# Optimization experiments

Hardware: AMD Instinct MI355X
Metric: run time of the kernel (lower is better)

The kernel has to match this reference:

```python
import jax, jax.numpy as jnp
import numpy as np

B, S, H, D = 2, 4096, 32, 128  # batch, seq_len, num_heads, key_size
BLOCK = 128                     # block_size (S must be divisible)


def setup_inputs() -> dict:
    key = jax.random.key(0)
    kq, kk, kv = jax.random.split(key, 3)
    q = jax.random.normal(kq, (B, S, H * D), dtype=jnp.float32)
    k = jax.random.normal(kk, (B, S, H * D), dtype=jnp.float32)
    v = jax.random.normal(kv, (B, S, H * D), dtype=jnp.float32)
    return {"q": q, "k": k, "v": v}


def reference(q, k, v):
    batch, seq_len, _ = q.shape
    nb = seq_len // BLOCK  # num_blocks
    # reshape to [B, nb, block, H, D]
    qb = q.reshape(batch, nb, BLOCK, H, D)
    kb = k.reshape(batch, nb, BLOCK, H, D)
    vb = v.reshape(batch, nb, BLOCK, H, D)
    scale = np.float32(1.0 / np.sqrt(D))
    # Faithful to original einsum '...hd,...kd->...hk': contraction is over d
    # with (nb, block) as batch dims, so attention runs over the HEAD axis (g).
    logits = jnp.einsum("bnshd,bnsgd->bnshg", qb, kb) * scale  # [B,nb,block,H,H]
    w = jax.nn.softmax(logits, axis=-1)
    out = jnp.einsum("bnshg,bnsgd->bnshd", w, vb)  # [B,nb,block,H,D]
    return out.reshape(batch, seq_len, H * D)
```

## Files before the change

kernel.cpp:

```cpp
#include <hip/hip_runtime.h>


typedef __bf16 bf16x8 __attribute__((ext_vector_type(8)));
typedef __bf16 bf16x2 __attribute__((ext_vector_type(2)));
typedef float  f32x4  __attribute__((ext_vector_type(4)));

static constexpr float kScale = 0.08838834764831845f;

typedef const __attribute__((address_space(1))) unsigned int* gas_ptr;
typedef __attribute__((address_space(3))) unsigned int* las_ptr;

__device__ inline bf16x8 to_bf16x8(f32x4 a, f32x4 b) {
  bf16x8 f;
  f[0] = (__bf16)a[0]; f[1] = (__bf16)a[1];
  f[2] = (__bf16)a[2]; f[3] = (__bf16)a[3];
  f[4] = (__bf16)b[0]; f[5] = (__bf16)b[1];
  f[6] = (__bf16)b[2]; f[7] = (__bf16)b[3];
  return f;
}

__global__ __launch_bounds__(256, 2) void attn_headwise(
    const float* __restrict__ q, const float* __restrict__ k,
    const float* __restrict__ v, float* __restrict__ out, int ntok) {
  const int wave = threadIdx.x >> 6;
  const int lane = threadIdx.x & 63;
  const int lr   = lane & 15;
  const int G    = lane >> 4;

  const long token = (long)blockIdx.x * 4 + wave;
  if (token >= ntok) return;
  const float* qt = q + token * 4096;
  const float* kt = k + token * 4096;
  const float* vt = v + token * 4096;
  float*       ot = out + token * 4096;

  __shared__ __align__(16) float        vbuf[4][32 * 128];
  __shared__ __align__(16) unsigned int pbuf[4][32 * 16];
  float*        vl = vbuf[wave];
  unsigned int* pl = pbuf[wave];

  f32x4 kraw[4][2][2], qraw[4][2][2];
  #pragma unroll
  for (int kk = 0; kk < 4; ++kk)
    #pragma unroll
    for (int t = 0; t < 2; ++t) {
      const float* pk = kt + (16 * t + lr) * 128 + 32 * kk + 8 * G;
      kraw[kk][t][0] = *(const f32x4*)pk;
      kraw[kk][t][1] = *(const f32x4*)(pk + 4);
      const float* pq = qt + (16 * t + lr) * 128 + 32 * kk + 8 * G;
      qraw[kk][t][0] = *(const f32x4*)pq;
      qraw[kk][t][1] = *(const f32x4*)(pq + 4);
    }

  {
    const float* vsrc = vt + lane * 4;
    #pragma unroll
    for (int i = 0; i < 16; ++i)
      __builtin_amdgcn_global_load_lds((gas_ptr)(vsrc + i * 256),
                                       (las_ptr)(vl + i * 256), 16, 0, 0);
  }

  f32x4 acc[2][2];
  acc[0][0] = 0.f; acc[0][1] = 0.f; acc[1][0] = 0.f; acc[1][1] = 0.f;
  #pragma unroll
  for (int kk = 0; kk < 4; ++kk) {
    bf16x8 af[2], bq[2];
    #pragma unroll
    for (int t = 0; t < 2; ++t) {
      af[t] = to_bf16x8(kraw[kk][t][0], kraw[kk][t][1]);
      bq[t] = to_bf16x8(qraw[kk][t][0], qraw[kk][t][1]);
    }
    #pragma unroll
    for (int gi = 0; gi < 2; ++gi)
      #pragma unroll
      for (int hj = 0; hj < 2; ++hj)
        acc[gi][hj] = __builtin_amdgcn_mfma_f32_16x16x32_bf16(
            af[gi], bq[hj], acc[gi][hj], 0, 0, 0);
  }

  #pragma unroll
  for (int hj = 0; hj < 2; ++hj) {
    float m = acc[0][hj][0];
    #pragma unroll
    for (int gi = 0; gi < 2; ++gi)
      #pragma unroll
      for (int r = 0; r < 4; ++r) m = fmaxf(m, acc[gi][hj][r]);
    m = fmaxf(m, __shfl_xor(m, 16, 64));
    m = fmaxf(m, __shfl_xor(m, 32, 64));

    float pv[2][4];
    float s = 0.f;
    #pragma unroll
    for (int gi = 0; gi < 2; ++gi)
      #pragma unroll
      for (int r = 0; r < 4; ++r) {
        float e = __expf((acc[gi][hj][r] - m) * kScale);
        pv[gi][r] = e;
        s += e;
      }
    s += __shfl_xor(s, 16, 64);
    s += __shfl_xor(s, 32, 64);
    float inv = 1.0f / s;

    #pragma unroll
    for (int gi = 0; gi < 2; ++gi)
      #pragma unroll
      for (int mp = 0; mp < 2; ++mp) {
        bf16x2 t;
        t[0] = (__bf16)(pv[gi][2 * mp]     * inv);
        t[1] = (__bf16)(pv[gi][2 * mp + 1] * inv);
        pl[(16 * hj + lr) * 16 + 8 * gi + 2 * G + mp] =
            __builtin_bit_cast(unsigned int, t);
      }
  }

  bf16x8 pf[2];
  #pragma unroll
  for (int ht = 0; ht < 2; ++ht)
    pf[ht] = *(const bf16x8*)&pl[(16 * ht + lr) * 16 + 4 * G];

  asm volatile("s_waitcnt vmcnt(0)" ::: "memory");
  f32x4 zero = 0.f;
  #pragma unroll
  for (int dt = 0; dt < 8; ++dt) {
    bf16x8 vf;
    #pragma unroll
    for (int e = 0; e < 8; ++e)
      vf[e] = (__bf16)vl[(8 * G + e) * 128 + 16 * dt + lr];
    f32x4 o0 = __builtin_amdgcn_mfma_f32_16x16x32_bf16(vf, pf[0], zero, 0, 0, 0);
    f32x4 o1 = __builtin_amdgcn_mfma_f32_16x16x32_bf16(vf, pf[1], zero, 0, 0, 0);
    *(f32x4*)&ot[lr * 128 + 16 * dt + 4 * G]        = o0;
    *(f32x4*)&ot[(16 + lr) * 128 + 16 * dt + 4 * G] = o1;
  }
}

extern "C" void kernel_launch(void* const* d_in, const int* in_sizes, int n_in,
                              void* d_out, int out_size, void* d_ws, size_t ws_size,
                              hipStream_t stream) {
  const float* q = (const float*)d_in[0];
  const float* k = (const float*)d_in[1];
  const float* v = (const float*)d_in[2];
  float* out = (float*)d_out;
  int ntok = in_sizes[0] / 4096;
  int grid = (ntok + 3) / 4;
  hipLaunchKernelGGL(attn_headwise, dim3(grid), dim3(256), 0, stream,
                     q, k, v, out, ntok);
}
```

Before: 113.3 us.

## Process multiple tokens per wave with register double-buffered prefetch

Each wave now handles several tokens in a grid-strided loop. While the current token is computed, it prefetches the next token's Q/K and V into registers, with sched_barriers placed so the loads overlap the MFMA and softmax work. V no longer goes through LDS via global_load_lds. Instead it is read straight into registers with scalar-per-element loads, and the P buffer row stride is padded to 20 to cut bank conflicts. The register footprint grows a lot (double-buffered raw fp32 Q/K/V), which risks spilling or lower occupancy, and the V loads become strided 4-byte accesses that coalesce less well.

```diff
diff --git a/kernel.cpp b/kernel.cpp
--- a/kernel.cpp
+++ b/kernel.cpp
@@ -6,9 +6,7 @@
 typedef float  f32x4  __attribute__((ext_vector_type(4)));
 
 static constexpr float kScale = 0.08838834764831845f;
-
-typedef const __attribute__((address_space(1))) unsigned int* gas_ptr;
-typedef __attribute__((address_space(3))) unsigned int* las_ptr;
+static constexpr int kTPW = 4;
 
 __device__ inline bf16x8 to_bf16x8(f32x4 a, f32x4 b) {
   bf16x8 f;
@@ -26,111 +24,133 @@
   const int lane = threadIdx.x & 63;
   const int lr   = lane & 15;
   const int G    = lane >> 4;
+  const int NW   = gridDim.x * 4;
+  const long wid = (long)blockIdx.x * 4 + wave;
 
-  const long token = (long)blockIdx.x * 4 + wave;
-  if (token >= ntok) return;
-  const float* qt = q + token * 4096;
-  const float* kt = k + token * 4096;
-  const float* vt = v + token * 4096;
-  float*       ot = out + token * 4096;
-
-  __shared__ __align__(16) float        vbuf[4][32 * 128];
-  __shared__ __align__(16) unsigned int pbuf[4][32 * 16];
-  float*        vl = vbuf[wave];
+  __shared__ __align__(16) unsigned int pbuf[4][32 * 20];
   unsigned int* pl = pbuf[wave];
 
-  f32x4 kraw[4][2][2], qraw[4][2][2];
-  #pragma unroll
-  for (int kk = 0; kk < 4; ++kk)
+  f32x4 kraw[2][4][2][2], qraw[2][4][2][2];
+  float vraw[2][8][8];
+
+  auto loadQK = [&](int buf, long t) {
+    const float* kt = k + t * 4096;
+    const float* qt = q + t * 4096;
     #pragma unroll
-    for (int t = 0; t < 2; ++t) {
-      const float* pk = kt + (16 * t + lr) * 128 + 32 * kk + 8 * G;
-      kraw[kk][t][0] = *(const f32x4*)pk;
-      kraw[kk][t][1] = *(const f32x4*)(pk + 4);
-      const float* pq = qt + (16 * t + lr) * 128 + 32 * kk + 8 * G;
-      qraw[kk][t][0] = *(const f32x4*)pq;
-      qraw[kk][t][1] = *(const f32x4*)(pq + 4);
-    }
+    for (int kk = 0; kk < 4; ++kk)
+      #pragma unroll
+      for (int tt = 0; tt < 2; ++tt) {
+        const float* pk = kt + (16 * tt + lr) * 128 + 32 * kk + 8 * G;
+        kraw[buf][kk][tt][0] = *(const f32x4*)pk;
+        kraw[buf][kk][tt][1] = *(const f32x4*)(pk + 4);
+        const float* pq = qt + (16 * tt + lr) * 128 + 32 * kk + 8 * G;
+        qraw[buf][kk][tt][0] = *(const f32x4*)pq;
+        qraw[buf][kk][tt][1] = *(const f32x4*)(pq + 4);
+      }
+  };
+  auto loadV = [&](int buf, long t) {
+    const float* vt = v + t * 4096;
+    #pragma unroll
+    for (int dt = 0; dt < 8; ++dt)
+      #pragma unroll
+      for (int e = 0; e < 8; ++e)
+        vraw[buf][dt][e] = vt[(8 * G + e) * 128 + 16 * dt + lr];
+  };
 
-  {
-    const float* vsrc = vt + lane * 4;
-    #pragma unroll
-    for (int i = 0; i < 16; ++i)
-      __builtin_amdgcn_global_load_lds((gas_ptr)(vsrc + i * 256),
-                                       (las_ptr)(vl + i * 256), 16, 0, 0);
-  }
-
-  f32x4 acc[2][2];
-  acc[0][0] = 0.f; acc[0][1] = 0.f; acc[1][0] = 0.f; acc[1][1] = 0.f;
-  #pragma unroll
-  for (int kk = 0; kk < 4; ++kk) {
-    bf16x8 af[2], bq[2];
-    #pragma unroll
-    for (int t = 0; t < 2; ++t) {
-      af[t] = to_bf16x8(kraw[kk][t][0], kraw[kk][t][1]);
-      bq[t] = to_bf16x8(qraw[kk][t][0], qraw[kk][t][1]);
-    }
-    #pragma unroll
-    for (int gi = 0; gi < 2; ++gi)
-      #pragma unroll
-      for (int hj = 0; hj < 2; ++hj)
-        acc[gi][hj] = __builtin_amdgcn_mfma_f32_16x16x32_bf16(
-            af[gi], bq[hj], acc[gi][hj], 0, 0, 0);
-  }
+  long tok = wid;
+  if (tok < ntok) { loadQK(0, tok); loadV(0, tok); }
 
   #pragma unroll
-  for (int hj = 0; hj < 2; ++hj) {
-    float m = acc[0][hj][0];
-    #pragma unroll
-    for (int gi = 0; gi < 2; ++gi)
+  for (int it = 0; it < kTPW; ++it) {
+    const int cur = it & 1, nxt = cur ^ 1;
+    const long tn = tok + NW;
+    if (tok < ntok) {
+      float* ot = out + tok * 4096;
+
+      bf16x8 kf[4][2], qf[4][2];
       #pragma unroll
-      for (int r = 0; r < 4; ++r) m = fmaxf(m, acc[gi][hj][r]);
-    m = fmaxf(m, __shfl_xor(m, 16, 64));
-    m = fmaxf(m, __shfl_xor(m, 32, 64));
+      for (int kk = 0; kk < 4; ++kk)
+        #pragma unroll
+        for (int tt = 0; tt < 2; ++tt) {
+          kf[kk][tt] = to_bf16x8(kraw[cur][kk][tt][0], kraw[cur][kk][tt][1]);
+          qf[kk][tt] = to_bf16x8(qraw[cur][kk][tt][0], qraw[cur][kk][tt][1]);
+        }
 
-    float pv[2][4];
-    float s = 0.f;
-    #pragma unroll
-    for (int gi = 0; gi < 2; ++gi)
+      bf16x8 vf[8];
       #pragma unroll
-      for (int r = 0; r < 4; ++r) {
-        float e = __expf((acc[gi][hj][r] - m) * kScale);
-        pv[gi][r] = e;
-        s += e;
+      for (int dt = 0; dt < 8; ++dt)
+        #pragma unroll
+        for (int e = 0; e < 8; ++e)
+          vf[dt][e] = (__bf16)vraw[cur][dt][e];
+
+      if (it + 1 < kTPW && tn < ntok) loadQK(nxt, tn);
+      __builtin_amdgcn_sched_barrier(0);
+
+      f32x4 acc[2][2];
+      acc[0][0] = 0.f; acc[0][1] = 0.f; acc[1][0] = 0.f; acc[1][1] = 0.f;
+      #pragma unroll
+      for (int kk = 0; kk < 4; ++kk)
+        #pragma unroll
+        for (int gi = 0; gi < 2; ++gi)
+          #pragma unroll
+          for (int hj = 0; hj < 2; ++hj)
+            acc[gi][hj] = __builtin_amdgcn_mfma_f32_16x16x32_bf16(
+                kf[kk][gi], qf[kk][hj], acc[gi][hj], 0, 0, 0);
+
+      #pragma unroll
+      for (int hj = 0; hj < 2; ++hj) {
+        float m = acc[0][hj][0];
+        #pragma unroll
+        for (int gi = 0; gi < 2; ++gi)
+          #pragma unroll
+          for (int r = 0; r < 4; ++r) m = fmaxf(m, acc[gi][hj][r]);
+        m = fmaxf(m, __shfl_xor(m, 16, 64));
+        m = fmaxf(m, __shfl_xor(m, 32, 64));
+
+        float pv[2][4];
+        float s = 0.f;
+        #pragma unroll
+        for (int gi = 0; gi < 2; ++gi)
+          #pragma unroll
+          for (int r = 0; r < 4; ++r) {
+            float e = __expf((acc[gi][hj][r] - m) * kScale);
+            pv[gi][r] = e;
+            s += e;
+          }
+        s += __shfl_xor(s, 16, 64);
+        s += __shfl_xor(s, 32, 64);
+        float inv = 1.0f / s;
+
+        #pragma unroll
+        for (int gi = 0; gi < 2; ++gi)
+          #pragma unroll
+          for (int mp = 0; mp < 2; ++mp) {
+            bf16x2 t2;
+            t2[0] = (__bf16)(pv[gi][2 * mp]     * inv);
+            t2[1] = (__bf16)(pv[gi][2 * mp + 1] * inv);
+            pl[(16 * hj + lr) * 20 + 8 * gi + 2 * G + mp] =
+                __builtin_bit_cast(unsigned int, t2);
+          }
       }
-    s += __shfl_xor(s, 16, 64);
-    s += __shfl_xor(s, 32, 64);
-    float inv = 1.0f / s;
 
-    #pragma unroll
-    for (int gi = 0; gi < 2; ++gi)
+      bf16x8 pf[2];
       #pragma unroll
-      for (int mp = 0; mp < 2; ++mp) {
-        bf16x2 t;
-        t[0] = (__bf16)(pv[gi][2 * mp]     * inv);
-        t[1] = (__bf16)(pv[gi][2 * mp + 1] * inv);
-        pl[(16 * hj + lr) * 16 + 8 * gi + 2 * G + mp] =
-            __builtin_bit_cast(unsigned int, t);
+      for (int ht = 0; ht < 2; ++ht)
+        pf[ht] = *(const bf16x8*)&pl[(16 * ht + lr) * 20 + 4 * G];
+
+      if (it + 1 < kTPW && tn < ntok) loadV(nxt, tn);
+      __builtin_amdgcn_sched_barrier(0);
+
+      f32x4 zero = 0.f;
+      #pragma unroll
+      for (int dt = 0; dt < 8; ++dt) {
+        f32x4 o0 = __builtin_amdgcn_mfma_f32_16x16x32_bf16(vf[dt], pf[0], zero, 0, 0, 0);
+        f32x4 o1 = __builtin_amdgcn_mfma_f32_16x16x32_bf16(vf[dt], pf[1], zero, 0, 0, 0);
+        *(f32x4*)&ot[lr * 128 + 16 * dt + 4 * G]        = o0;
+        *(f32x4*)&ot[(16 + lr) * 128 + 16 * dt + 4 * G] = o1;
       }
-  }
-
-  bf16x8 pf[2];
-  #pragma unroll
-  for (int ht = 0; ht < 2; ++ht)
-    pf[ht] = *(const bf16x8*)&pl[(16 * ht + lr) * 16 + 4 * G];
-
-  asm volatile("s_waitcnt vmcnt(0)" ::: "memory");
-  f32x4 zero = 0.f;
-  #pragma unroll
-  for (int dt = 0; dt < 8; ++dt) {
-    bf16x8 vf;
-    #pragma unroll
-    for (int e = 0; e < 8; ++e)
-      vf[e] = (__bf16)vl[(8 * G + e) * 128 + 16 * dt + lr];
-    f32x4 o0 = __builtin_amdgcn_mfma_f32_16x16x32_bf16(vf, pf[0], zero, 0, 0, 0);
-    f32x4 o1 = __builtin_amdgcn_mfma_f32_16x16x32_bf16(vf, pf[1], zero, 0, 0, 0);
-    *(f32x4*)&ot[lr * 128 + 16 * dt + 4 * G]        = o0;
-    *(f32x4*)&ot[(16 + lr) * 128 + 16 * dt + 4 * G] = o1;
+    }
+    tok = tn;
   }
 }
 
@@ -142,7 +162,7 @@
   const float* v = (const float*)d_in[2];
   float* out = (float*)d_out;
   int ntok = in_sizes[0] / 4096;
-  int grid = (ntok + 3) / 4;
+  int grid = (ntok + 4 * kTPW - 1) / (4 * kTPW);
   hipLaunchKernelGGL(attn_headwise, dim3(grid), dim3(256), 0, stream,
                      q, k, v, out, ntok);
 }
```

Result: slower. 289.8 us (+155.7%).

## Pipeline four tokens per single-wave block with double-buffered V prefetch

Applied to the files above, without the earlier changes.

Each block becomes a single wave that handles four consecutive tokens in sequence. While the current token's softmax and PV product run, the next token's Q and K are prefetched into registers and its V into a second LDS buffer, with a partial vmcnt wait so those loads overlap compute. The aim is to hide global-load latency in what is essentially a bandwidth-bound kernel. The P scratch row stride is padded to 20 words to reduce LDS bank conflicts. The cost is fewer resident waves per CU, because of the larger per-wave LDS footprint and 64-thread blocks, which may reduce latency hiding from occupancy.

```diff
diff --git a/kernel.cpp b/kernel.cpp
--- a/kernel.cpp
+++ b/kernel.cpp
@@ -6,6 +6,7 @@
 typedef float  f32x4  __attribute__((ext_vector_type(4)));
 
 static constexpr float kScale = 0.08838834764831845f;
+static constexpr int kTPW = 4;
 
 typedef const __attribute__((address_space(1))) unsigned int* gas_ptr;
 typedef __attribute__((address_space(3))) unsigned int* las_ptr;
@@ -19,118 +20,137 @@
   return f;
 }
 
-__global__ __launch_bounds__(256, 2) void attn_headwise(
+__global__ __launch_bounds__(64) void attn_headwise(
     const float* __restrict__ q, const float* __restrict__ k,
     const float* __restrict__ v, float* __restrict__ out, int ntok) {
-  const int wave = threadIdx.x >> 6;
-  const int lane = threadIdx.x & 63;
+  const int lane = threadIdx.x;
   const int lr   = lane & 15;
   const int G    = lane >> 4;
+  const long base = (long)blockIdx.x * kTPW;
 
-  const long token = (long)blockIdx.x * 4 + wave;
-  if (token >= ntok) return;
-  const float* qt = q + token * 4096;
-  const float* kt = k + token * 4096;
-  const float* vt = v + token * 4096;
-  float*       ot = out + token * 4096;
-
-  __shared__ __align__(16) float        vbuf[4][32 * 128];
-  __shared__ __align__(16) unsigned int pbuf[4][32 * 16];
-  float*        vl = vbuf[wave];
-  unsigned int* pl = pbuf[wave];
+  __shared__ __align__(16) float        vbuf[2][32 * 128];
+  __shared__ __align__(16) unsigned int pbuf[32 * 20];
 
   f32x4 kraw[4][2][2], qraw[4][2][2];
-  #pragma unroll
-  for (int kk = 0; kk < 4; ++kk)
+
+  auto clampTok = [&](long t) { return t < (long)ntok ? t : (long)ntok - 1; };
+
+  auto issueQK = [&](long t) {
+    const float* kt = k + t * 4096;
+    const float* qt = q + t * 4096;
     #pragma unroll
-    for (int t = 0; t < 2; ++t) {
-      const float* pk = kt + (16 * t + lr) * 128 + 32 * kk + 8 * G;
-      kraw[kk][t][0] = *(const f32x4*)pk;
-      kraw[kk][t][1] = *(const f32x4*)(pk + 4);
-      const float* pq = qt + (16 * t + lr) * 128 + 32 * kk + 8 * G;
-      qraw[kk][t][0] = *(const f32x4*)pq;
-      qraw[kk][t][1] = *(const f32x4*)(pq + 4);
-    }
-
-  {
-    const float* vsrc = vt + lane * 4;
+    for (int kk = 0; kk < 4; ++kk)
+      #pragma unroll
+      for (int tt = 0; tt < 2; ++tt) {
+        const float* pk = kt + (16 * tt + lr) * 128 + 32 * kk + 8 * G;
+        kraw[kk][tt][0] = *(const f32x4*)pk;
+        kraw[kk][tt][1] = *(const f32x4*)(pk + 4);
+        const float* pq = qt + (16 * tt + lr) * 128 + 32 * kk + 8 * G;
+        qraw[kk][tt][0] = *(const f32x4*)pq;
+        qraw[kk][tt][1] = *(const f32x4*)(pq + 4);
+      }
+  };
+  auto issueV = [&](long t, int buf) {
+    const float* vsrc = v + t * 4096 + lane * 4;
+    float*       vdst = vbuf[buf];
     #pragma unroll
     for (int i = 0; i < 16; ++i)
       __builtin_amdgcn_global_load_lds((gas_ptr)(vsrc + i * 256),
-                                       (las_ptr)(vl + i * 256), 16, 0, 0);
-  }
+                                       (las_ptr)(vdst + i * 256), 16, 0, 0);
+  };
 
-  f32x4 acc[2][2];
-  acc[0][0] = 0.f; acc[0][1] = 0.f; acc[1][0] = 0.f; acc[1][1] = 0.f;
-  #pragma unroll
-  for (int kk = 0; kk < 4; ++kk) {
-    bf16x8 af[2], bq[2];
-    #pragma unroll
-    for (int t = 0; t < 2; ++t) {
-      af[t] = to_bf16x8(kraw[kk][t][0], kraw[kk][t][1]);
-      bq[t] = to_bf16x8(qraw[kk][t][0], qraw[kk][t][1]);
-    }
-    #pragma unroll
-    for (int gi = 0; gi < 2; ++gi)
-      #pragma unroll
-      for (int hj = 0; hj < 2; ++hj)
-        acc[gi][hj] = __builtin_amdgcn_mfma_f32_16x16x32_bf16(
-            af[gi], bq[hj], acc[gi][hj], 0, 0, 0);
-  }
+  issueQK(clampTok(base));
+  issueV(clampTok(base), 0);
 
   #pragma unroll
-  for (int hj = 0; hj < 2; ++hj) {
-    float m = acc[0][hj][0];
+  for (int it = 0; it < kTPW; ++it) {
+    const long tok = clampTok(base + it);
+    float* ot = out + tok * 4096;
+
+    f32x4 acc[2][2];
+    acc[0][0] = 0.f; acc[0][1] = 0.f; acc[1][0] = 0.f; acc[1][1] = 0.f;
     #pragma unroll
-    for (int gi = 0; gi < 2; ++gi)
+    for (int kk = 0; kk < 4; ++kk) {
+      bf16x8 kf[2], qf[2];
       #pragma unroll
-      for (int r = 0; r < 4; ++r) m = fmaxf(m, acc[gi][hj][r]);
-    m = fmaxf(m, __shfl_xor(m, 16, 64));
-    m = fmaxf(m, __shfl_xor(m, 32, 64));
+      for (int tt = 0; tt < 2; ++tt) {
+        kf[tt] = to_bf16x8(kraw[kk][tt][0], kraw[kk][tt][1]);
+        qf[tt] = to_bf16x8(qraw[kk][tt][0], qraw[kk][tt][1]);
+      }
+      #pragma unroll
+      for (int gi = 0; gi < 2; ++gi)
+        #pragma unroll
+        for (int hj = 0; hj < 2; ++hj)
+          acc[gi][hj] = __builtin_amdgcn_mfma_f32_16x16x32_bf16(
+              kf[gi], qf[hj], acc[gi][hj], 0, 0, 0);
+    }
 
-    float pv[2][4];
-    float s = 0.f;
-    #pragma unroll
-    for (int gi = 0; gi < 2; ++gi)
-      #pragma unroll
-      for (int r = 0; r < 4; ++r) {
-        float e = __expf((acc[gi][hj][r] - m) * kScale);
-        pv[gi][r] = e;
-        s += e;
-      }
-    s += __shfl_xor(s, 16, 64);
-    s += __shfl_xor(s, 32, 64);
-    float inv = 1.0f / s;
+    if (it + 1 < kTPW) {
+      issueQK(clampTok(base + it + 1));
+      issueV(clampTok(base + it + 1), (it + 1) & 1);
+    }
+    __builtin_amdgcn_sched_barrier(0);
 
     #pragma unroll
-    for (int gi = 0; gi < 2; ++gi)
+    for (int hj = 0; hj < 2; ++hj) {
+      float m = acc[0][hj][0];
       #pragma unroll
-      for (int mp = 0; mp < 2; ++mp) {
-        bf16x2 t;
-        t[0] = (__bf16)(pv[gi][2 * mp]     * inv);
-        t[1] = (__bf16)(pv[gi][2 * mp + 1] * inv);
-        pl[(16 * hj + lr) * 16 + 8 * gi + 2 * G + mp] =
-            __builtin_bit_cast(unsigned int, t);
-      }
-  }
+      for (int gi = 0; gi < 2; ++gi)
+        #pragma unroll
+        for (int r = 0; r < 4; ++r) m = fmaxf(m, acc[gi][hj][r]);
+      m = fmaxf(m, __shfl_xor(m, 16, 64));
+      m = fmaxf(m, __shfl_xor(m, 32, 64));
 
-  bf16x8 pf[2];
-  #pragma unroll
-  for (int ht = 0; ht < 2; ++ht)
-    pf[ht] = *(const bf16x8*)&pl[(16 * ht + lr) * 16 + 4 * G];
+      float pv[2][4];
+      float s = 0.f;
+      #pragma unroll
+      for (int gi = 0; gi < 2; ++gi)
+        #pragma unroll
+        for (int r = 0; r < 4; ++r) {
+          float e = __expf((acc[gi][hj][r] - m) * kScale);
+          pv[gi][r] = e;
+          s += e;
+        }
+      s += __shfl_xor(s, 16, 64);
+      s += __shfl_xor(s, 32, 64);
+      float inv = 1.0f / s;
 
-  asm volatile("s_waitcnt vmcnt(0)" ::: "memory");
-  f32x4 zero = 0.f;
-  #pragma unroll
-  for (int dt = 0; dt < 8; ++dt) {
-    bf16x8 vf;
+      #pragma unroll
+      for (int gi = 0; gi < 2; ++gi)
+        #pragma unroll
+        for (int mp = 0; mp < 2; ++mp) {
+          bf16x2 t2;
+          t2[0] = (__bf16)(pv[gi][2 * mp]     * inv);
+          t2[1] = (__bf16)(pv[gi][2 * mp + 1] * inv);
+          pbuf[(16 * hj + lr) * 20 + 8 * gi + 2 * G + mp] =
+              __builtin_bit_cast(unsigned int, t2);
+        }
+    }
+    bf16x8 pf[2];
     #pragma unroll
-    for (int e = 0; e < 8; ++e)
-      vf[e] = (__bf16)vl[(8 * G + e) * 128 + 16 * dt + lr];
-    f32x4 o0 = __builtin_amdgcn_mfma_f32_16x16x32_bf16(vf, pf[0], zero, 0, 0, 0);
-    f32x4 o1 = __builtin_amdgcn_mfma_f32_16x16x32_bf16(vf, pf[1], zero, 0, 0, 0);
-    *(f32x4*)&ot[lr * 128 + 16 * dt + 4 * G]        = o0;
-    *(f32x4*)&ot[(16 + lr) * 128 + 16 * dt + 4 * G] = o1;
+    for (int ht = 0; ht < 2; ++ht)
+      pf[ht] = *(const bf16x8*)&pbuf[(16 * ht + lr) * 20 + 4 * G];
+
+    if (it + 1 < kTPW) {
+      asm volatile("s_waitcnt vmcnt(48)" ::: "memory");
+    } else {
+      asm volatile("s_waitcnt vmcnt(0)" ::: "memory");
+    }
+    __builtin_amdgcn_sched_barrier(0);
+
+    const float* vl = vbuf[it & 1];
+    f32x4 zero = 0.f;
+    #pragma unroll
+    for (int dt = 0; dt < 8; ++dt) {
+      bf16x8 vf;
+      #pragma unroll
+      for (int e = 0; e < 8; ++e)
+        vf[e] = (__bf16)vl[(8 * G + e) * 128 + 16 * dt + lr];
+      f32x4 o0 = __builtin_amdgcn_mfma_f32_16x16x32_bf16(vf, pf[0], zero, 0, 0, 0);
+      f32x4 o1 = __builtin_amdgcn_mfma_f32_16x16x32_bf16(vf, pf[1], zero, 0, 0, 0);
+      *(f32x4*)&ot[lr * 128 + 16 * dt + 4 * G]        = o0;
+      *(f32x4*)&ot[(16 + lr) * 128 + 16 * dt + 4 * G] = o1;
+    }
   }
 }
 
@@ -142,7 +162,7 @@
   const float* v = (const float*)d_in[2];
   float* out = (float*)d_out;
   int ntok = in_sizes[0] / 4096;
-  int grid = (ntok + 3) / 4;
-  hipLaunchKernelGGL(attn_headwise, dim3(grid), dim3(256), 0, stream,
+  int grid = (ntok + kTPW - 1) / kTPW;
+  hipLaunchKernelGGL(attn_headwise, dim3(grid), dim3(64), 0, stream,
                      q, k, v, out, ntok);
 }
```

New measurement: 117.2 us. +3.4%, slower.
